# Performance work log

Measured on AMD Instinct MI355X. Metric: run time of the kernel, lower is better.

## Reference

```python
import jax, jax.numpy as jnp
import numpy as np
from jax import lax

_SIGMA = 1.5
_KSIZE = 5
_THRESH = 30.0
# TF rgb_to_grayscale luma weights
_RGB_W = np.array([0.2989, 0.5870, 0.1140], dtype=np.float32)

def _gauss1d():
    x = np.arange(_KSIZE, dtype=np.float32) - (_KSIZE - 1) / 2.0
    g = np.exp(-(x ** 2) / (2.0 * _SIGMA ** 2))
    return (g / g.sum()).astype(np.float32)

def _conv2d_same(x, k2d):
    # x: [B,H,W,1], k2d: [kh,kw]; reflect padding (TF image-op convention), valid conv
    kh, kw = k2d.shape
    ph, pw = kh // 2, kw // 2
    xp = jnp.pad(x, ((0, 0), (ph, ph), (pw, pw), (0, 0)), mode='reflect')
    k = k2d.reshape(kh, kw, 1, 1)
    return lax.conv_general_dilated(xp, k, window_strides=(1, 1), padding='VALID',
                                    dimension_numbers=('NHWC', 'HWIO', 'NHWC'))

def setup_inputs() -> dict:
    key = jax.random.key(0)
    inputs = jax.random.uniform(key, (32, 512, 512, 3), dtype=jnp.float32)
    return {"inputs": inputs}

def reference(inputs):
    # 1) grayscale
    gray = jnp.einsum('bhwc,c->bhw', inputs, jnp.asarray(_RGB_W))[..., None]  # [B,H,W,1]
    # 2) 5x5 gaussian blur (separable)
    g1 = jnp.asarray(_gauss1d())
    blurred = _conv2d_same(gray, g1[:, None])   # vertical pass [5,1]
    blurred = _conv2d_same(blurred, g1[None, :])  # horizontal pass [1,5]
    # 3) sobel x / y (3x3)
    kx = jnp.asarray(np.array([[-1, 0, 1], [-2, 0, 2], [-1, 0, 1]], dtype=np.float32))
    ky = jnp.asarray(np.array([[-1, -2, -1], [0, 0, 0], [1, 2, 1]], dtype=np.float32))
    sx = _conv2d_same(blurred, kx)
    sy = _conv2d_same(blurred, ky)
    # 4) magnitude + threshold (direction computed then unused in original; skipped)
    magnitude = jnp.sqrt(sx * sx + sy * sy)
    edges = jnp.where(magnitude > _THRESH, 1.0, 0.0).astype(inputs.dtype)
    return edges
```

## Files before the change

### kernel.cpp

```cpp
#include <hip/hip_runtime.h>

#define IMG_H 512
#define IMG_W 512
#define TW 64
#define TH 32
#define GW 72
#define GH 38
#define GS 72
#define TMH 34
#define TMS 72
#define BH 34
#define BS 68

__device__ __forceinline__ int reflect(int i, int n) {
    i = (i < 0) ? -i : i;
    return (i >= n) ? (2 * n - 2 - i) : i;
}
__device__ __forceinline__ float4 ld4s(const float* p) { return *(const float4*)p; }
__device__ __forceinline__ ushort pkbf(float f) { return (ushort)(__builtin_bit_cast(unsigned, f) >> 16); }
__device__ __forceinline__ float  upbf(ushort u) { return __builtin_bit_cast(float, (unsigned)u << 16); }

#define GRAY4(v0, v1, v2, dst) do { \
    float4 g_; \
    g_.x = (v0).x * wr + (v0).y * wg + (v0).z * wb; \
    g_.y = (v0).w * wr + (v1).x * wg + (v1).y * wb; \
    g_.z = (v1).z * wr + (v1).w * wg + (v2).x * wb; \
    g_.w = (v2).y * wr + (v2).z * wg + (v2).w * wb; \
    *(float4*)(dst) = g_; \
} while (0)

__global__ __launch_bounds__(256, 8)
void edge_fused_kernel(const float* __restrict__ in, float* __restrict__ out) {
    const int bx0 = blockIdx.x * TW;
    const int by0 = blockIdx.y * TH;
    const int b   = blockIdx.z;
    const int tid = threadIdx.x;

    __shared__ float  A[GH * GS];
    __shared__ ushort Bf[TMH * TMS + 8];

    const float kg0 = 0.12007838f, kg1 = 0.23388076f, kg2 = 0.29208171f;
    const float wr = 0.2989f, wg = 0.5870f, wb = 0.1140f;

    const float* img = in + (size_t)b * (IMG_H * IMG_W * 3);
    const int gx0 = bx0 - 4;
    const bool left  = (bx0 == 0);
    const bool right = (bx0 + TW == IMG_W);

    if (!left && !right) {
        const int idxA = tid, idxB = tid + 256, idxC = tid + 512;
        const int iA = idxA / 18, jA = idxA % 18;
        const int iB = idxB / 18, jB = idxB % 18;
        const int iC = idxC / 18, jC = idxC % 18;
        const bool hasC = (idxC < GH * 18);
        const float* rpA = img + (size_t)reflect(by0 - 3 + iA, IMG_H) * (IMG_W * 3) + (gx0 + 4 * jA) * 3;
        const float* rpB = img + (size_t)reflect(by0 - 3 + iB, IMG_H) * (IMG_W * 3) + (gx0 + 4 * jB) * 3;
        const float4 a0 = ld4s(rpA), a1 = ld4s(rpA + 4), a2 = ld4s(rpA + 8);
        const float4 b0 = ld4s(rpB), b1 = ld4s(rpB + 4), b2 = ld4s(rpB + 8);
        GRAY4(a0, a1, a2, &A[iA * GS + 4 * jA]);
        float4 c0, c1, c2;
        if (hasC) {
            const float* rpC = img + (size_t)reflect(by0 - 3 + iC, IMG_H) * (IMG_W * 3) + (gx0 + 4 * jC) * 3;
            c0 = ld4s(rpC); c1 = ld4s(rpC + 4); c2 = ld4s(rpC + 8);
        }
        GRAY4(b0, b1, b2, &A[iB * GS + 4 * jB]);
        if (hasC) GRAY4(c0, c1, c2, &A[iC * GS + 4 * jC]);
    } else {
        const int go = left ? 1 : 0;
        for (int idx = tid; idx < GH * 17; idx += 256) {
            const int i = idx / 17, g = idx % 17 + go;
            const int gy = reflect(by0 - 3 + i, IMG_H);
            const float* rp = img + (size_t)gy * (IMG_W * 3) + (gx0 + 4 * g) * 3;
            const float4 v0 = ld4s(rp), v1 = ld4s(rp + 4), v2 = ld4s(rp + 8);
            GRAY4(v0, v1, v2, &A[i * GS + 4 * g]);
        }
        const int jbase = left ? 0 : 68;
        for (int idx = tid; idx < GH * 4; idx += 256) {
            const int i = idx / 4, j = idx % 4;
            const int gy = reflect(by0 - 3 + i, IMG_H);
            const int gx = reflect(gx0 + jbase + j, IMG_W);
            const float* p = img + (size_t)gy * (IMG_W * 3) + gx * 3;
            A[i * GS + jbase + j] = p[0] * wr + p[1] * wg + p[2] * wb;
        }
    }
    __syncthreads();

    for (int idx = tid; idx < TMH * 18; idx += 256) {
        const int i = idx / 18, g = idx % 18;
        const float* c = &A[i * GS + 4 * g];
        const float4 r0 = ld4s(c);
        const float4 r1 = ld4s(c + GS);
        const float4 r2 = ld4s(c + 2 * GS);
        const float4 r3 = ld4s(c + 3 * GS);
        const float4 r4 = ld4s(c + 4 * GS);
        ushort4 u;
        u.x = pkbf(kg0 * (r0.x + r4.x) + kg1 * (r1.x + r3.x) + kg2 * r2.x);
        u.y = pkbf(kg0 * (r0.y + r4.y) + kg1 * (r1.y + r3.y) + kg2 * r2.y);
        u.z = pkbf(kg0 * (r0.z + r4.z) + kg1 * (r1.z + r3.z) + kg2 * r2.z);
        u.w = pkbf(kg0 * (r0.w + r4.w) + kg1 * (r1.w + r3.w) + kg2 * r2.w);
        *(ushort4*)&Bf[i * TMS + 4 * g] = u;
    }
    __syncthreads();

    for (int idx = tid; idx < BH * 17; idx += 256) {
        const int i = idx / 17, g = idx % 17;
        const ushort* c = &Bf[i * TMS + 4 * g];
        const ushort4 ua = *(const ushort4*)c;
        const ushort4 ub = *(const ushort4*)(c + 4);
        const float a1 = upbf(ua.y), a2 = upbf(ua.z), a3 = upbf(ua.w);
        const float d0 = upbf(ub.x), d1 = upbf(ub.y), d2 = upbf(ub.z), d3 = upbf(ub.w);
        const float e0 = upbf(c[8]);
        float4 o;
        o.x = kg0 * (a1 + d1) + kg1 * (a2 + d0) + kg2 * a3;
        o.y = kg0 * (a2 + d2) + kg1 * (a3 + d1) + kg2 * d0;
        o.z = kg0 * (a3 + d3) + kg1 * (d0 + d2) + kg2 * d1;
        o.w = kg0 * (d0 + e0) + kg1 * (d1 + d3) + kg2 * d2;
        *(float4*)&A[i * BS + 4 * g] = o;
    }
    __syncthreads();

    const int x = (tid & 15) * 4;
    float* ob = out + (size_t)b * (IMG_H * IMG_W) + (size_t)by0 * IMG_W + bx0;
    #pragma unroll
    for (int yy = 0; yy < 2; ++yy) {
        const int y = (tid >> 4) + 16 * yy;
        const float* r0 = &A[y * BS + x];
        float t[8], m[8], bo[8];
        float4 q;
        q = ld4s(r0);            t[0]=q.x; t[1]=q.y; t[2]=q.z; t[3]=q.w;
        q = ld4s(r0 + 4);        t[4]=q.x; t[5]=q.y; t[6]=q.z; t[7]=q.w;
        q = ld4s(r0 + BS);       m[0]=q.x; m[1]=q.y; m[2]=q.z; m[3]=q.w;
        q = ld4s(r0 + BS + 4);   m[4]=q.x; m[5]=q.y; m[6]=q.z; m[7]=q.w;
        q = ld4s(r0 + 2*BS);     bo[0]=q.x; bo[1]=q.y; bo[2]=q.z; bo[3]=q.w;
        q = ld4s(r0 + 2*BS + 4); bo[4]=q.x; bo[5]=q.y; bo[6]=q.z; bo[7]=q.w;
        float res[4];
        #pragma unroll
        for (int k = 0; k < 4; ++k) {
            const float tl = t[k],  tc = t[k+1],  tr = t[k+2];
            const float ml = m[k],                 mr = m[k+2];
            const float bl = bo[k], bc = bo[k+1], br = bo[k+2];
            const float sx = (tr - tl) + 2.0f * (mr - ml) + (br - bl);
            const float sy = (bl - tl) + 2.0f * (bc - tc) + (br - tr);
            const float m2 = sx * sx + sy * sy;
            res[k] = (m2 > 900.0f) ? 1.0f : 0.0f;
        }
        float4 rv; rv.x = res[0]; rv.y = res[1]; rv.z = res[2]; rv.w = res[3];
        *(float4*)&ob[(size_t)y * IMG_W + x] = rv;
    }
}

extern "C" void kernel_launch(void* const* d_in, const int* in_sizes, int n_in,
                              void* d_out, int out_size, void* d_ws, size_t ws_size,
                              hipStream_t stream) {
    const float* in = (const float*)d_in[0];
    float* out = (float*)d_out;
    const int B = in_sizes[0] / (IMG_H * IMG_W * 3);
    dim3 grid(IMG_W / TW, IMG_H / TH, B);
    dim3 block(256, 1, 1);
    edge_fused_kernel<<<grid, block, 0, stream>>>(in, out);
}
```

Baseline: 153.6 us.

## Fold Gaussian into Sobel as separable 7-tap filters with bf16 grayscale tile

Combines the 5-tap Gaussian with the 3x3 Sobel into composite 7-tap separable kernels: one vertical pass produces smoothing and derivative intermediates, and a horizontal pass finishes sx and sy. This removes one shared-memory stage and one barrier, and the grayscale tile is now stored as bf16 to halve shared-memory footprint and traffic. The cost is more FMAs per output and bf16 rounding at the grayscale stage, which could flip pixels near the threshold. The reflect padding is no longer applied between the blur and Sobel stages, so edge handling at image borders may differ from the reference.

```diff
diff --git a/kernel.cpp b/kernel.cpp
--- a/kernel.cpp
+++ b/kernel.cpp
@@ -4,13 +4,9 @@
 #define IMG_W 512
 #define TW 64
 #define TH 32
-#define GW 72
 #define GH 38
-#define GS 72
-#define TMH 34
-#define TMS 72
-#define BH 34
-#define BS 68
+#define AS 72
+#define VS 72
 
 __device__ __forceinline__ int reflect(int i, int n) {
     i = (i < 0) ? -i : i;
@@ -20,13 +16,13 @@
 __device__ __forceinline__ ushort pkbf(float f) { return (ushort)(__builtin_bit_cast(unsigned, f) >> 16); }
 __device__ __forceinline__ float  upbf(ushort u) { return __builtin_bit_cast(float, (unsigned)u << 16); }
 
-#define GRAY4(v0, v1, v2, dst) do { \
-    float4 g_; \
-    g_.x = (v0).x * wr + (v0).y * wg + (v0).z * wb; \
-    g_.y = (v0).w * wr + (v1).x * wg + (v1).y * wb; \
-    g_.z = (v1).z * wr + (v1).w * wg + (v2).x * wb; \
-    g_.w = (v2).y * wr + (v2).z * wg + (v2).w * wb; \
-    *(float4*)(dst) = g_; \
+#define GRAY4U(v0, v1, v2, dst) do { \
+    ushort4 g_; \
+    g_.x = pkbf((v0).x * wr + (v0).y * wg + (v0).z * wb); \
+    g_.y = pkbf((v0).w * wr + (v1).x * wg + (v1).y * wb); \
+    g_.z = pkbf((v1).z * wr + (v1).w * wg + (v2).x * wb); \
+    g_.w = pkbf((v2).y * wr + (v2).z * wg + (v2).w * wb); \
+    *(ushort4*)(dst) = g_; \
 } while (0)
 
 __global__ __launch_bounds__(256, 8)
@@ -36,10 +32,18 @@
     const int b   = blockIdx.z;
     const int tid = threadIdx.x;
 
-    __shared__ float  A[GH * GS];
-    __shared__ ushort Bf[TMH * TMS + 8];
+    __shared__ ushort A[GH * AS];
+    __shared__ ushort B1[TH * VS];
+    __shared__ ushort B2[TH * VS];
 
-    const float kg0 = 0.12007838f, kg1 = 0.23388076f, kg2 = 0.29208171f;
+    const float g0 = 0.12007838f, g1 = 0.23388076f, g2 = 0.29208171f;
+    const float c0 = 1.05192494f;
+    const float c1 = 0.87992161f;
+    const float c2 = 0.47403752f;
+    const float c3 = 0.12007838f;
+    const float a1 = 0.17200333f;
+    const float a2 = 0.23388076f;
+    const float a3 = 0.12007838f;
     const float wr = 0.2989f, wg = 0.5870f, wb = 0.1140f;
 
     const float* img = in + (size_t)b * (IMG_H * IMG_W * 3);
@@ -55,16 +59,16 @@
         const bool hasC = (idxC < GH * 18);
         const float* rpA = img + (size_t)reflect(by0 - 3 + iA, IMG_H) * (IMG_W * 3) + (gx0 + 4 * jA) * 3;
         const float* rpB = img + (size_t)reflect(by0 - 3 + iB, IMG_H) * (IMG_W * 3) + (gx0 + 4 * jB) * 3;
-        const float4 a0 = ld4s(rpA), a1 = ld4s(rpA + 4), a2 = ld4s(rpA + 8);
-        const float4 b0 = ld4s(rpB), b1 = ld4s(rpB + 4), b2 = ld4s(rpB + 8);
-        GRAY4(a0, a1, a2, &A[iA * GS + 4 * jA]);
-        float4 c0, c1, c2;
+        const float4 a0 = ld4s(rpA), a1v = ld4s(rpA + 4), a2v = ld4s(rpA + 8);
+        const float4 b0 = ld4s(rpB), b1v = ld4s(rpB + 4), b2v = ld4s(rpB + 8);
+        GRAY4U(a0, a1v, a2v, &A[iA * AS + 4 * jA]);
+        float4 q0, q1, q2;
         if (hasC) {
             const float* rpC = img + (size_t)reflect(by0 - 3 + iC, IMG_H) * (IMG_W * 3) + (gx0 + 4 * jC) * 3;
-            c0 = ld4s(rpC); c1 = ld4s(rpC + 4); c2 = ld4s(rpC + 8);
+            q0 = ld4s(rpC); q1 = ld4s(rpC + 4); q2 = ld4s(rpC + 8);
         }
-        GRAY4(b0, b1, b2, &A[iB * GS + 4 * jB]);
-        if (hasC) GRAY4(c0, c1, c2, &A[iC * GS + 4 * jC]);
+        GRAY4U(b0, b1v, b2v, &A[iB * AS + 4 * jB]);
+        if (hasC) GRAY4U(q0, q1, q2, &A[iC * AS + 4 * jC]);
     } else {
         const int go = left ? 1 : 0;
         for (int idx = tid; idx < GH * 17; idx += 256) {
@@ -72,7 +76,7 @@
             const int gy = reflect(by0 - 3 + i, IMG_H);
             const float* rp = img + (size_t)gy * (IMG_W * 3) + (gx0 + 4 * g) * 3;
             const float4 v0 = ld4s(rp), v1 = ld4s(rp + 4), v2 = ld4s(rp + 8);
-            GRAY4(v0, v1, v2, &A[i * GS + 4 * g]);
+            GRAY4U(v0, v1, v2, &A[i * AS + 4 * g]);
         }
         const int jbase = left ? 0 : 68;
         for (int idx = tid; idx < GH * 4; idx += 256) {
@@ -80,72 +84,72 @@
             const int gy = reflect(by0 - 3 + i, IMG_H);
             const int gx = reflect(gx0 + jbase + j, IMG_W);
             const float* p = img + (size_t)gy * (IMG_W * 3) + gx * 3;
-            A[i * GS + jbase + j] = p[0] * wr + p[1] * wg + p[2] * wb;
+            A[i * AS + jbase + j] = pkbf(p[0] * wr + p[1] * wg + p[2] * wb);
         }
     }
     __syncthreads();
 
-    for (int idx = tid; idx < TMH * 18; idx += 256) {
-        const int i = idx / 18, g = idx % 18;
-        const float* c = &A[i * GS + 4 * g];
-        const float4 r0 = ld4s(c);
-        const float4 r1 = ld4s(c + GS);
-        const float4 r2 = ld4s(c + 2 * GS);
-        const float4 r3 = ld4s(c + 3 * GS);
-        const float4 r4 = ld4s(c + 4 * GS);
-        ushort4 u;
-        u.x = pkbf(kg0 * (r0.x + r4.x) + kg1 * (r1.x + r3.x) + kg2 * r2.x);
-        u.y = pkbf(kg0 * (r0.y + r4.y) + kg1 * (r1.y + r3.y) + kg2 * r2.y);
-        u.z = pkbf(kg0 * (r0.z + r4.z) + kg1 * (r1.z + r3.z) + kg2 * r2.z);
-        u.w = pkbf(kg0 * (r0.w + r4.w) + kg1 * (r1.w + r3.w) + kg2 * r2.w);
-        *(ushort4*)&Bf[i * TMS + 4 * g] = u;
+    {
+        const float C1[7] = { c3, c2, c1, c0, c1, c2, c3 };
+        const float C2[7] = { -a3, -a2, -a1, 0.0f, a1, a2, a3 };
+        for (int t = 0; t < 3; ++t) {
+            const int idx = tid + 256 * t;
+            if (idx >= TH * 18) break;
+            const int r = idx / 18, g = idx % 18;
+            const ushort* base = &A[r * AS + 4 * g];
+            float v1x = 0, v1y = 0, v1z = 0, v1w = 0;
+            float v2x = 0, v2y = 0, v2z = 0, v2w = 0;
+            #pragma unroll
+            for (int k = 0; k < 7; ++k) {
+                const ushort4 xq = *(const ushort4*)(base + k * AS);
+                const float x0 = upbf(xq.x), x1 = upbf(xq.y), x2 = upbf(xq.z), x3 = upbf(xq.w);
+                v1x = fmaf(C1[k], x0, v1x); v1y = fmaf(C1[k], x1, v1y);
+                v1z = fmaf(C1[k], x2, v1z); v1w = fmaf(C1[k], x3, v1w);
+                if (k != 3) {
+                    v2x = fmaf(C2[k], x0, v2x); v2y = fmaf(C2[k], x1, v2y);
+                    v2z = fmaf(C2[k], x2, v2z); v2w = fmaf(C2[k], x3, v2w);
+                }
+            }
+            ushort4 o1, o2;
+            o1.x = pkbf(v1x); o1.y = pkbf(v1y); o1.z = pkbf(v1z); o1.w = pkbf(v1w);
+            o2.x = pkbf(v2x); o2.y = pkbf(v2y); o2.z = pkbf(v2z); o2.w = pkbf(v2w);
+            *(ushort4*)&B1[r * VS + 4 * g] = o1;
+            *(ushort4*)&B2[r * VS + 4 * g] = o2;
+        }
     }
     __syncthreads();
 
-    for (int idx = tid; idx < BH * 17; idx += 256) {
-        const int i = idx / 17, g = idx % 17;
-        const ushort* c = &Bf[i * TMS + 4 * g];
-        const ushort4 ua = *(const ushort4*)c;
-        const ushort4 ub = *(const ushort4*)(c + 4);
-        const float a1 = upbf(ua.y), a2 = upbf(ua.z), a3 = upbf(ua.w);
-        const float d0 = upbf(ub.x), d1 = upbf(ub.y), d2 = upbf(ub.z), d3 = upbf(ub.w);
-        const float e0 = upbf(c[8]);
-        float4 o;
-        o.x = kg0 * (a1 + d1) + kg1 * (a2 + d0) + kg2 * a3;
-        o.y = kg0 * (a2 + d2) + kg1 * (a3 + d1) + kg2 * d0;
-        o.z = kg0 * (a3 + d3) + kg1 * (d0 + d2) + kg2 * d1;
-        o.w = kg0 * (d0 + e0) + kg1 * (d1 + d3) + kg2 * d2;
-        *(float4*)&A[i * BS + 4 * g] = o;
-    }
-    __syncthreads();
-
-    const int x = (tid & 15) * 4;
-    float* ob = out + (size_t)b * (IMG_H * IMG_W) + (size_t)by0 * IMG_W + bx0;
     #pragma unroll
-    for (int yy = 0; yy < 2; ++yy) {
-        const int y = (tid >> 4) + 16 * yy;
-        const float* r0 = &A[y * BS + x];
-        float t[8], m[8], bo[8];
-        float4 q;
-        q = ld4s(r0);            t[0]=q.x; t[1]=q.y; t[2]=q.z; t[3]=q.w;
-        q = ld4s(r0 + 4);        t[4]=q.x; t[5]=q.y; t[6]=q.z; t[7]=q.w;
-        q = ld4s(r0 + BS);       m[0]=q.x; m[1]=q.y; m[2]=q.z; m[3]=q.w;
-        q = ld4s(r0 + BS + 4);   m[4]=q.x; m[5]=q.y; m[6]=q.z; m[7]=q.w;
-        q = ld4s(r0 + 2*BS);     bo[0]=q.x; bo[1]=q.y; bo[2]=q.z; bo[3]=q.w;
-        q = ld4s(r0 + 2*BS + 4); bo[4]=q.x; bo[5]=q.y; bo[6]=q.z; bo[7]=q.w;
+    for (int t = 0; t < 2; ++t) {
+        const int idx = tid + 256 * t;
+        const int r = idx >> 4, g = idx & 15;
+        const ushort* p1 = &B1[r * VS + 4 * g];
+        const ushort* p2 = &B2[r * VS + 4 * g];
+        const ushort4 ua = *(const ushort4*)p1;
+        const ushort4 ub = *(const ushort4*)(p1 + 4);
+        const ushort4 uc = *(const ushort4*)(p1 + 8);
+        const ushort4 wa = *(const ushort4*)p2;
+        const ushort4 wb2 = *(const ushort4*)(p2 + 4);
+        const ushort4 wc = *(const ushort4*)(p2 + 8);
+        float u[12], w[12];
+        u[0]=upbf(ua.x); u[1]=upbf(ua.y); u[2]=upbf(ua.z); u[3]=upbf(ua.w);
+        u[4]=upbf(ub.x); u[5]=upbf(ub.y); u[6]=upbf(ub.z); u[7]=upbf(ub.w);
+        u[8]=upbf(uc.x); u[9]=upbf(uc.y); u[10]=upbf(uc.z); u[11]=upbf(uc.w);
+        w[0]=upbf(wa.x); w[1]=upbf(wa.y); w[2]=upbf(wa.z); w[3]=upbf(wa.w);
+        w[4]=upbf(wb2.x); w[5]=upbf(wb2.y); w[6]=upbf(wb2.z); w[7]=upbf(wb2.w);
+        w[8]=upbf(wc.x); w[9]=upbf(wc.y); w[10]=upbf(wc.z); w[11]=upbf(wc.w);
         float res[4];
         #pragma unroll
-        for (int k = 0; k < 4; ++k) {
-            const float tl = t[k],  tc = t[k+1],  tr = t[k+2];
-            const float ml = m[k],                 mr = m[k+2];
-            const float bl = bo[k], bc = bo[k+1], br = bo[k+2];
-            const float sx = (tr - tl) + 2.0f * (mr - ml) + (br - bl);
-            const float sy = (bl - tl) + 2.0f * (bc - tc) + (br - tr);
+        for (int p = 0; p < 4; ++p) {
+            const int j = p + 4;
+            const float sx = (u[j+3] - u[j-3]) * a3 + (u[j+2] - u[j-2]) * a2 + (u[j+1] - u[j-1]) * a1;
+            const float sy = c0 * w[j] + c1 * (w[j-1] + w[j+1]) + c2 * (w[j-2] + w[j+2]) + c3 * (w[j-3] + w[j+3]);
             const float m2 = sx * sx + sy * sy;
-            res[k] = (m2 > 900.0f) ? 1.0f : 0.0f;
+            res[p] = (m2 > 900.0f) ? 1.0f : 0.0f;
         }
         float4 rv; rv.x = res[0]; rv.y = res[1]; rv.z = res[2]; rv.w = res[3];
-        *(float4*)&ob[(size_t)y * IMG_W + x] = rv;
+        float* ob = out + (size_t)b * (IMG_H * IMG_W) + (size_t)(by0 + r) * IMG_W + bx0 + 4 * g;
+        *(float4*)ob = rv;
     }
 }
 
```

Result: no change. 155.3 us (+1.1%).
